# Optimization experiments

Measured on AMD Instinct MI355X. Metric: run time of the kernel, lower is better.

## Reference

```python
import jax, jax.numpy as jnp
import numpy as np

B, S, D, E = 4, 4096, 2048, 8


def setup_inputs() -> dict:
    key = jax.random.key(0)
    kx, kw, kb = jax.random.split(key, 3)
    x = jax.random.normal(kx, (B, S, D), dtype=jnp.float32)
    # nn.Linear(d_model, n_experts): weight [E, D], bias [E]
    bound = 1.0 / np.sqrt(D)
    W = jax.random.uniform(kw, (E, D), minval=-bound, maxval=bound, dtype=jnp.float32)
    b = jax.random.uniform(kb, (E,), minval=-bound, maxval=bound, dtype=jnp.float32)
    return {"x": x, "W": W, "b": b}


def reference(x, W, b):
    # logits = x @ W^T + b : [B, S, E]
    logits = jnp.einsum("bsd,ed->bse", x, W) + b
    gate = jax.nn.softmax(logits, axis=-1)
    top2_val, top2_idx = jax.lax.top_k(gate, 2)  # [B, S, 2] each
    return (top2_val, top2_idx, gate)
```

## Files before the change

kernel.cpp:

```cpp
#include <hip/hip_runtime.h>
#include <hip/hip_bf16.h>
#include <math.h>


#define NTOK  16384
#define DM    2048
#define NE    8
#define TPB   16
#define KQ    512

typedef float v4f __attribute__((ext_vector_type(4)));

__device__ __forceinline__ float fold4(const float4 a) {
    return (a.x + a.y) + (a.z + a.w);
}

__device__ __forceinline__ float reduce_scatter8(const float4* acc, const int j) {
    float v0 = fold4(acc[0]), v1 = fold4(acc[1]), v2 = fold4(acc[2]), v3 = fold4(acc[3]);
    float v4 = fold4(acc[4]), v5 = fold4(acc[5]), v6 = fold4(acc[6]), v7 = fold4(acc[7]);
    float s0 = v0 + __shfl_xor(v0, 1, 8);
    float s1 = v1 + __shfl_xor(v1, 1, 8);
    float s2 = v2 + __shfl_xor(v2, 1, 8);
    float s3 = v3 + __shfl_xor(v3, 1, 8);
    float s4 = v4 + __shfl_xor(v4, 1, 8);
    float s5 = v5 + __shfl_xor(v5, 1, 8);
    float s6 = v6 + __shfl_xor(v6, 1, 8);
    float s7 = v7 + __shfl_xor(v7, 1, 8);
    const bool b0 = (j & 1);
    float t0 = b0 ? s1 : s0;
    float t1 = b0 ? s3 : s2;
    float t2 = b0 ? s5 : s4;
    float t3 = b0 ? s7 : s6;
    float p0 = t0 + __shfl_xor(t0, 2, 8);
    float p1 = t1 + __shfl_xor(t1, 2, 8);
    float p2 = t2 + __shfl_xor(t2, 2, 8);
    float p3 = t3 + __shfl_xor(t3, 2, 8);
    const bool b1 = (j & 2);
    float u0 = b1 ? p1 : p0;
    float u1 = b1 ? p3 : p2;
    float q0 = u0 + __shfl_xor(u0, 4, 8);
    float q1 = u1 + __shfl_xor(u1, 4, 8);
    return (j & 4) ? q1 : q0;
}

__device__ __forceinline__ void softmax_top2(const float logit, const int j,
                                             const int token, float* __restrict__ out) {
    float m = logit;
#pragma unroll
    for (int s = 4; s; s >>= 1) m = fmaxf(m, __shfl_xor(m, s, 8));
    const float ex = expf(logit - m);
    float sum = ex;
#pragma unroll
    for (int s = 4; s; s >>= 1) sum += __shfl_xor(sum, s, 8);
    const float gate = ex / sum;

    out[65536 + token * NE + j] = gate;

    float g1 = gate; int e1 = j;
#pragma unroll
    for (int s = 4; s; s >>= 1) {
        const float og = __shfl_xor(g1, s, 8);
        const int   oe = __shfl_xor(e1, s, 8);
        if (og > g1 || (og == g1 && oe < e1)) { g1 = og; e1 = oe; }
    }
    float g2 = (j == e1) ? -INFINITY : gate; int e2 = j;
#pragma unroll
    for (int s = 4; s; s >>= 1) {
        const float og = __shfl_xor(g2, s, 8);
        const int   oe = __shfl_xor(e2, s, 8);
        if (og > g2 || (og == g2 && oe < e2)) { g2 = og; e2 = oe; }
    }
    if (j == 0) {
        out[token * 2 + 0]         = g1;
        out[token * 2 + 1]         = g2;
        out[32768 + token * 2 + 0] = (float)e1;
        out[32768 + token * 2 + 1] = (float)e2;
    }
}

__global__ __launch_bounds__(256, 2) void router_fused(
    const float* __restrict__ x,
    const float* __restrict__ W,
    const float* __restrict__ b,
    float* __restrict__ out)
{
    __shared__ __align__(16) float sWq[4 * NE * KQ];
    __shared__ float sPart[4 * TPB * NE];

    const int t    = threadIdx.x;
    const int wv   = t >> 6;
    const int lane = t & 63;
    const int j    = lane & 7;
    const int st   = lane >> 3;

    {
        const float4* __restrict__ Wv = reinterpret_cast<const float4*>(W);
        float4* sWv = reinterpret_cast<float4*>(&sWq[wv * NE * KQ]);
#pragma unroll
        for (int i = 0; i < 16; ++i) {
            const int L  = i * 64 + lane;
            const int e  = L >> 7;
            const int f4 = L & 127;
            sWv[L] = Wv[e * (DM / 4) + wv * (KQ / 4) + f4];
        }
    }

    const int tokbase = blockIdx.x * TPB;
    const int tok0 = tokbase + st;
    const int tok1 = tokbase + st + 8;
    const float* __restrict__ xp0 = x + (size_t)tok0 * DM + wv * KQ + (j << 2);
    const float* __restrict__ xp1 = x + (size_t)tok1 * DM + wv * KQ + (j << 2);

    float4 acc0[NE], acc1[NE];
#pragma unroll
    for (int e = 0; e < NE; ++e) {
        acc0[e] = make_float4(0.f, 0.f, 0.f, 0.f);
        acc1[e] = make_float4(0.f, 0.f, 0.f, 0.f);
    }

    v4f xa0 = __builtin_nontemporal_load(reinterpret_cast<const v4f*>(xp0));
    v4f xa1 = __builtin_nontemporal_load(reinterpret_cast<const v4f*>(xp1));
#pragma unroll
    for (int it = 0; it < 16; ++it) {
        v4f xn0, xn1;
        if (it < 15) {
            xn0 = __builtin_nontemporal_load(
                reinterpret_cast<const v4f*>(xp0 + ((it + 1) << 5)));
            xn1 = __builtin_nontemporal_load(
                reinterpret_cast<const v4f*>(xp1 + ((it + 1) << 5)));
        }
        const float* wbase = &sWq[wv * NE * KQ + (it << 5) + (j << 2)];
#pragma unroll
        for (int e = 0; e < NE; ++e) {
            const float4 wvv = *reinterpret_cast<const float4*>(wbase + e * KQ);
            acc0[e].x = fmaf(xa0.x, wvv.x, acc0[e].x);
            acc0[e].y = fmaf(xa0.y, wvv.y, acc0[e].y);
            acc0[e].z = fmaf(xa0.z, wvv.z, acc0[e].z);
            acc0[e].w = fmaf(xa0.w, wvv.w, acc0[e].w);
            acc1[e].x = fmaf(xa1.x, wvv.x, acc1[e].x);
            acc1[e].y = fmaf(xa1.y, wvv.y, acc1[e].y);
            acc1[e].z = fmaf(xa1.z, wvv.z, acc1[e].z);
            acc1[e].w = fmaf(xa1.w, wvv.w, acc1[e].w);
        }
        xa0 = xn0;
        xa1 = xn1;
    }

    const float p0 = reduce_scatter8(acc0, j);
    const float p1 = reduce_scatter8(acc1, j);
    sPart[wv * (TPB * NE) + st * NE + j]       = p0;
    sPart[wv * (TPB * NE) + (st + 8) * NE + j] = p1;
    __syncthreads();

    if (wv < 2) {
        const int tk   = wv * 8 + st;
        const int gtok = tokbase + tk;
        float s = sPart[0 * (TPB * NE) + tk * NE + j]
                + sPart[1 * (TPB * NE) + tk * NE + j]
                + sPart[2 * (TPB * NE) + tk * NE + j]
                + sPart[3 * (TPB * NE) + tk * NE + j];
        const float logit = s + b[j];
        softmax_top2(logit, j, gtok, out);
    }
}

extern "C" void kernel_launch(void* const* d_in, const int* in_sizes, int n_in,
                              void* d_out, int out_size, void* d_ws, size_t ws_size,
                              hipStream_t stream) {
    const float* x = (const float*)d_in[0];
    const float* W = (const float*)d_in[1];
    const float* b = (const float*)d_in[2];
    float* out = (float*)d_out;

    router_fused<<<NTOK / TPB, 256, 0, stream>>>(x, W, b, out);
}
```

Measured before the change: 183.7 us.

## Process four token groups per lane to raise W reuse per block

Doubles tokens per block from 16 to 32 so each thread accumulates four tokens instead of two, reusing each shared-memory W float4 load across more FMAs and halving the number of blocks that stage W into LDS. All four waves now run the softmax/top-2 epilogue. In exchange, register pressure roughly doubles (128 accumulator floats plus prefetch buffers), which may lower occupancy under launch_bounds(256,2) or cause spills.

```diff
diff --git a/kernel.cpp b/kernel.cpp
--- a/kernel.cpp
+++ b/kernel.cpp
@@ -6,8 +6,9 @@
 #define NTOK  16384
 #define DM    2048
 #define NE    8
-#define TPB   16
+#define TPB   32
 #define KQ    512
+#define TG    4
 
 typedef float v4f __attribute__((ext_vector_type(4)));
 
@@ -106,53 +107,57 @@
     }
 
     const int tokbase = blockIdx.x * TPB;
-    const int tok0 = tokbase + st;
-    const int tok1 = tokbase + st + 8;
-    const float* __restrict__ xp0 = x + (size_t)tok0 * DM + wv * KQ + (j << 2);
-    const float* __restrict__ xp1 = x + (size_t)tok1 * DM + wv * KQ + (j << 2);
 
-    float4 acc0[NE], acc1[NE];
+    const float* __restrict__ xp[TG];
 #pragma unroll
-    for (int e = 0; e < NE; ++e) {
-        acc0[e] = make_float4(0.f, 0.f, 0.f, 0.f);
-        acc1[e] = make_float4(0.f, 0.f, 0.f, 0.f);
-    }
+    for (int g = 0; g < TG; ++g)
+        xp[g] = x + (size_t)(tokbase + st + 8 * g) * DM + wv * KQ + (j << 2);
 
-    v4f xa0 = __builtin_nontemporal_load(reinterpret_cast<const v4f*>(xp0));
-    v4f xa1 = __builtin_nontemporal_load(reinterpret_cast<const v4f*>(xp1));
+    float4 acc[TG][NE];
+#pragma unroll
+    for (int g = 0; g < TG; ++g)
+#pragma unroll
+        for (int e = 0; e < NE; ++e)
+            acc[g][e] = make_float4(0.f, 0.f, 0.f, 0.f);
+
+    v4f xa[TG];
+#pragma unroll
+    for (int g = 0; g < TG; ++g)
+        xa[g] = __builtin_nontemporal_load(reinterpret_cast<const v4f*>(xp[g]));
+
 #pragma unroll
     for (int it = 0; it < 16; ++it) {
-        v4f xn0, xn1;
+        v4f xn[TG];
         if (it < 15) {
-            xn0 = __builtin_nontemporal_load(
-                reinterpret_cast<const v4f*>(xp0 + ((it + 1) << 5)));
-            xn1 = __builtin_nontemporal_load(
-                reinterpret_cast<const v4f*>(xp1 + ((it + 1) << 5)));
+#pragma unroll
+            for (int g = 0; g < TG; ++g)
+                xn[g] = __builtin_nontemporal_load(
+                    reinterpret_cast<const v4f*>(xp[g] + ((it + 1) << 5)));
         }
         const float* wbase = &sWq[wv * NE * KQ + (it << 5) + (j << 2)];
 #pragma unroll
         for (int e = 0; e < NE; ++e) {
             const float4 wvv = *reinterpret_cast<const float4*>(wbase + e * KQ);
-            acc0[e].x = fmaf(xa0.x, wvv.x, acc0[e].x);
-            acc0[e].y = fmaf(xa0.y, wvv.y, acc0[e].y);
-            acc0[e].z = fmaf(xa0.z, wvv.z, acc0[e].z);
-            acc0[e].w = fmaf(xa0.w, wvv.w, acc0[e].w);
-            acc1[e].x = fmaf(xa1.x, wvv.x, acc1[e].x);
-            acc1[e].y = fmaf(xa1.y, wvv.y, acc1[e].y);
-            acc1[e].z = fmaf(xa1.z, wvv.z, acc1[e].z);
-            acc1[e].w = fmaf(xa1.w, wvv.w, acc1[e].w);
+#pragma unroll
+            for (int g = 0; g < TG; ++g) {
+                acc[g][e].x = fmaf(xa[g].x, wvv.x, acc[g][e].x);
+                acc[g][e].y = fmaf(xa[g].y, wvv.y, acc[g][e].y);
+                acc[g][e].z = fmaf(xa[g].z, wvv.z, acc[g][e].z);
+                acc[g][e].w = fmaf(xa[g].w, wvv.w, acc[g][e].w);
+            }
         }
-        xa0 = xn0;
-        xa1 = xn1;
+#pragma unroll
+        for (int g = 0; g < TG; ++g) xa[g] = xn[g];
     }
 
-    const float p0 = reduce_scatter8(acc0, j);
-    const float p1 = reduce_scatter8(acc1, j);
-    sPart[wv * (TPB * NE) + st * NE + j]       = p0;
-    sPart[wv * (TPB * NE) + (st + 8) * NE + j] = p1;
+#pragma unroll
+    for (int g = 0; g < TG; ++g) {
+        const float p = reduce_scatter8(acc[g], j);
+        sPart[wv * (TPB * NE) + (st + 8 * g) * NE + j] = p;
+    }
     __syncthreads();
 
-    if (wv < 2) {
+    {
         const int tk   = wv * 8 + st;
         const int gtok = tokbase + tk;
         float s = sPart[0 * (TPB * NE) + tk * NE + j]
```

Result: no change. 181.8 us (-1.0%).
